# Optimization experiments

Measured on AMD Instinct MI355X. Metric: run time of the kernel, lower is better.

## Reference

```python
import jax, jax.numpy as jnp
import numpy as np
import math

# SS2D (VMamba v2) config
D_MODEL = 96
D_INNER = 192          # ssm_ratio * d_model (== d_expand, ssm_rank_ratio==ssm_ratio)
D_STATE = 16
DT_RANK = 6            # ceil(96/16)
K = 4                  # scan directions
D_CONV = 3
STEP = 2               # EfficientScan step_size
BATCH, H, W = 4, 64, 64  # H,W chosen even -> no padding branch
LN_EPS = 1e-5


def efficient_scan(x):
    # x: (B, C, H, W) with H,W divisible by STEP -> (B, 4, C, (H/2)*(W/2))
    Bn, C = x.shape[0], x.shape[1]
    xt = jnp.swapaxes(x, 2, 3)  # (B, C, W, H)
    xs0 = x[:, :, ::STEP, ::STEP].reshape(Bn, C, -1)
    xs1 = xt[:, :, ::STEP, 1::STEP].reshape(Bn, C, -1)
    xs2 = x[:, :, ::STEP, 1::STEP].reshape(Bn, C, -1)
    xs3 = xt[:, :, 1::STEP, 1::STEP].reshape(Bn, C, -1)
    return jnp.stack([xs0, xs1, xs2, xs3], axis=1)


def efficient_merge(ys, ori_h, ori_w):
    # ys: (B, 4, C, L') -> (B, C, ori_h*ori_w)
    Bn, _, C, _ = ys.shape
    Hs, Ws = ori_h // STEP, ori_w // STEP
    a = ys[:, 0].reshape(Bn, C, Hs, Ws)
    b = jnp.swapaxes(ys[:, 1].reshape(Bn, C, Ws, Hs), 2, 3)
    c = ys[:, 2].reshape(Bn, C, Hs, Ws)
    d = jnp.swapaxes(ys[:, 3].reshape(Bn, C, Ws, Hs), 2, 3)
    y = jnp.zeros((Bn, C, ori_h, ori_w), ys.dtype)
    y = y.at[:, :, ::STEP, ::STEP].set(a)
    y = y.at[:, :, 1::STEP, ::STEP].set(b)
    y = y.at[:, :, ::STEP, 1::STEP].set(c)
    y = y.at[:, :, 1::STEP, 1::STEP].set(d)
    return y.reshape(Bn, C, ori_h * ori_w)


def selective_scan(u, delta, A, Bs, Cs, D, delta_bias):
    # u, delta: (B, K*Dg, L); A: (K*Dg, N); Bs, Cs: (B, K, N, L); D, delta_bias: (K*Dg,)
    Bn, KD, L = u.shape
    N = A.shape[1]
    Dg = KD // K
    delta = jax.nn.softplus(delta + delta_bias[None, :, None])
    u4 = u.reshape(Bn, K, Dg, L)
    dt4 = delta.reshape(Bn, K, Dg, L)
    A4 = A.reshape(K, Dg, N)
    # discretized transition / input, time-major for scan: (L, B, K, Dg, N)
    dA = jnp.exp(jnp.einsum('bkdl,kdn->lbkdn', dt4, A4))
    dBu = jnp.einsum('bkdl,bknl,bkdl->lbkdn', dt4, Bs, u4)

    def step(h, inp):
        dA_t, dBu_t = inp
        h = dA_t * h + dBu_t
        return h, h

    h0 = jnp.zeros((Bn, K, Dg, N), u.dtype)
    _, hs = jax.lax.scan(step, h0, (dA, dBu))  # (L, B, K, Dg, N)
    y = jnp.einsum('lbkdn,bknl->bkdl', hs, Cs)
    y = y + u4 * D.reshape(1, K, Dg, 1)
    return y.reshape(Bn, KD, L)


def setup_inputs() -> dict:
    key = jax.random.key(0)
    ks = jax.random.split(key, 10)
    f = jnp.float32
    x = jax.random.normal(ks[0], (BATCH, H, W, D_MODEL), f)
    W_in = jax.random.normal(ks[1], (2 * D_INNER, D_MODEL), f) / math.sqrt(D_MODEL)
    conv_w = jax.random.normal(ks[2], (D_INNER, 1, D_CONV, D_CONV), f) / math.sqrt(D_CONV * D_CONV)
    conv_b = jax.random.normal(ks[3], (D_INNER,), f) * 0.01
    x_proj_weight = jax.random.normal(ks[4], (K, DT_RANK + 2 * D_STATE, D_INNER), f) / math.sqrt(D_INNER)
    dt_projs_weight = jax.random.normal(ks[5], (K, D_INNER, DT_RANK), f) / math.sqrt(DT_RANK)
    dt_projs_bias = jax.random.normal(ks[6], (K, D_INNER), f) * 0.1
    A_logs = jnp.log(jnp.tile(jnp.arange(1, D_STATE + 1, dtype=f), (K * D_INNER, 1)))
    Ds = jnp.ones((K * D_INNER,), f)
    ln_g = jnp.ones((D_INNER,), f)
    ln_b = jnp.zeros((D_INNER,), f)
    W_out = jax.random.normal(ks[7], (D_MODEL, D_INNER), f) / math.sqrt(D_INNER)
    return dict(x=x, W_in=W_in, conv_w=conv_w, conv_b=conv_b,
                x_proj_weight=x_proj_weight, dt_projs_weight=dt_projs_weight,
                dt_projs_bias=dt_projs_bias, A_logs=A_logs, Ds=Ds,
                ln_g=ln_g, ln_b=ln_b, W_out=W_out)


def _ss2d_forward(x, W_in, conv_w, conv_b, x_proj_weight, dt_projs_weight,
                  dt_projs_bias, A_logs, Ds, ln_g, ln_b, W_out):
    Bn = x.shape[0]
    # in_proj (no bias), split into x and gate z
    xz = jnp.einsum('bhwc,ec->bhwe', x, W_in)            # (B,H,W,2*D_INNER)
    xin, z = jnp.split(xz, 2, axis=-1)
    z = jax.nn.silu(z)
    # depthwise conv 3x3 (SAME) + SiLU, NCHW
    xc = jnp.transpose(xin, (0, 3, 1, 2))                 # (B, D_INNER, H, W)
    xc = jax.lax.conv_general_dilated(
        xc, conv_w, window_strides=(1, 1), padding=((1, 1), (1, 1)),
        feature_group_count=D_INNER,
        dimension_numbers=('NCHW', 'OIHW', 'NCHW')) + conv_b[None, :, None, None]
    xc = jax.nn.silu(xc)
    # cross_selective_scan
    xs = efficient_scan(xc)                               # (B, 4, C, L')
    Lp = xs.shape[-1]
    x_dbl = jnp.einsum('bkdl,kcd->bkcl', xs, x_proj_weight)
    dts, Bs, Cs = jnp.split(x_dbl, [DT_RANK, DT_RANK + D_STATE], axis=2)
    dts = jnp.einsum('bkrl,kdr->bkdl', dts, dt_projs_weight)
    u = xs.reshape(Bn, -1, Lp).astype(jnp.float32)
    delta = dts.reshape(Bn, -1, Lp).astype(jnp.float32)
    A = -jnp.exp(A_logs.astype(jnp.float32))
    ys = selective_scan(u, delta, A, Bs.astype(jnp.float32), Cs.astype(jnp.float32),
                        Ds.astype(jnp.float32), dt_projs_bias.reshape(-1).astype(jnp.float32))
    ys = ys.reshape(Bn, K, -1, Lp)
    y = efficient_merge(ys, H, W)                         # (B, C, H*W)
    y = jnp.swapaxes(y, 1, 2)                             # (B, L, C)
    # LayerNorm over channel dim
    mu = jnp.mean(y, axis=-1, keepdims=True)
    var = jnp.var(y, axis=-1, keepdims=True)
    y = (y - mu) * jax.lax.rsqrt(var + LN_EPS) * ln_g + ln_b
    y = y.reshape(Bn, H, W, D_INNER).astype(x.dtype)
    # gate and out_proj (no bias)
    y = y * z
    out = jnp.einsum('bhwd,od->bhwo', y, W_out)
    return out


def reference(x, W_in, conv_w, conv_b, x_proj_weight, dt_projs_weight,
              dt_projs_bias, A_logs, Ds, ln_g, ln_b, W_out):
    return _ss2d_forward(x, W_in, conv_w, conv_b, x_proj_weight, dt_projs_weight,
                         dt_projs_bias, A_logs, Ds, ln_g, ln_b, W_out)
```

## Files before the change

### kernel.cpp

```cpp
#include <hip/hip_runtime.h>
#include <math.h>


#define DINNER 192
#define NSTATE 16
#define KDIR 4
#define BATCH 4
#define NPIX (BATCH * 64 * 64)
#define LP 1024
#define NCH 128
#define CHUNK 8
#define NBK (BATCH * KDIR)
#define NSTATES (NBK * DINNER * NSTATE)
#define SSTRIDE (NBK * DINNER)
#define USTRIDE 196
#define GSTRIDE 200

typedef __attribute__((ext_vector_type(8))) short short8;
typedef __attribute__((ext_vector_type(4))) short short4v;
typedef __attribute__((ext_vector_type(4))) float f32x4;

__device__ __forceinline__ float silu_f(float x) {
    return x / (1.0f + __expf(-x));
}
__device__ __forceinline__ float softplus_f(float a) {
    return (a > 20.0f) ? a : __logf(1.0f + __expf(a));
}
__device__ __forceinline__ unsigned short f2bf(float f) {
    unsigned u = __float_as_uint(f);
    unsigned r = (u + 0x7FFFu + ((u >> 16) & 1u)) >> 16;
    return (unsigned short)r;
}
__device__ __forceinline__ float bf2f(unsigned short h) {
    return __uint_as_float(((unsigned)h) << 16);
}

__global__ __launch_bounds__(256) void k_castW(
        const float* __restrict__ W_in, const float* __restrict__ W_out,
        unsigned short* __restrict__ Wi_hi, unsigned short* __restrict__ Wi_lo,
        unsigned short* __restrict__ Wo_bf) {
    int i = blockIdx.x * 256 + threadIdx.x;
    if (i < 384 * 96) {
        float v = W_in[i];
        unsigned short h = f2bf(v);
        Wi_hi[i] = h;
        Wi_lo[i] = f2bf(v - bf2f(h));
    }
    if (i < 96 * DINNER) Wo_bf[i] = f2bf(W_out[i]);
}

__global__ __launch_bounds__(256) void k_inproj3(
        const float* __restrict__ x,
        const unsigned short* __restrict__ Wi_hi,
        const unsigned short* __restrict__ Wi_lo,
        float* __restrict__ xin, float* __restrict__ z) {
    int p0 = blockIdx.x * 16;
    int w = threadIdx.x >> 6;
    int lane = threadIdx.x & 63;
    int m = lane & 15, quad = lane >> 4;
    const short* wh = (const short*)Wi_hi;
    const short* wl = (const short*)Wi_lo;
    short8 ah[3], al[3];
    #pragma unroll
    for (int c = 0; c < 3; ++c) {
        const float* xr = x + (size_t)(p0 + m) * 96 + c * 32 + quad * 8;
        short8 hi, lo;
        #pragma unroll
        for (int j = 0; j < 8; ++j) {
            float v = xr[j];
            unsigned short hb = f2bf(v);
            hi[j] = (short)hb;
            lo[j] = (short)f2bf(v - bf2f(hb));
        }
        ah[c] = hi;
        al[c] = lo;
    }
    #pragma unroll
    for (int i = 0; i < 6; ++i) {
        int e0 = (w * 6 + i) * 16;
        f32x4 acc = {0.f, 0.f, 0.f, 0.f};
        #pragma unroll
        for (int c = 0; c < 3; ++c) {
            size_t o = (size_t)(e0 + m) * 96 + c * 32 + quad * 8;
            short8 bh = *(const short8*)(wh + o);
            short8 bl = *(const short8*)(wl + o);
            acc = __builtin_amdgcn_mfma_f32_16x16x32_bf16(ah[c], bl, acc, 0, 0, 0);
            acc = __builtin_amdgcn_mfma_f32_16x16x32_bf16(al[c], bh, acc, 0, 0, 0);
            acc = __builtin_amdgcn_mfma_f32_16x16x32_bf16(ah[c], bh, acc, 0, 0, 0);
        }
        int e = e0 + m;
        #pragma unroll
        for (int r = 0; r < 4; ++r) {
            int p = p0 + quad * 4 + r;
            if (e < 192) xin[(size_t)p * 192 + e] = acc[r];
            else         z[(size_t)p * 192 + (e - 192)] = silu_f(acc[r]);
        }
    }
}

__global__ __launch_bounds__(192) void k_conv8(
        const float* __restrict__ xin, const float* __restrict__ cw,
        const float* __restrict__ cb, float* __restrict__ xg) {
    int blk = blockIdx.x;
    int b = blk >> 9;
    int rem = blk & 511;
    int h = rem >> 3;
    int w0 = (rem & 7) * 8;
    int d = threadIdx.x;
    float wr[3][3];
    #pragma unroll
    for (int i = 0; i < 3; ++i)
        #pragma unroll
        for (int j = 0; j < 3; ++j) wr[i][j] = cw[d * 9 + i * 3 + j];
    float bias = cb[d];
    float acc[8];
    #pragma unroll
    for (int o = 0; o < 8; ++o) acc[o] = bias;
    #pragma unroll
    for (int jj = 0; jj < 10; ++jj) {
        int ww = w0 + jj - 1;
        float r0 = 0.0f, r1 = 0.0f, r2 = 0.0f;
        if ((unsigned)ww < 64u) {
            const float* base = xin + ((size_t)b * 4096 + h * 64 + ww) * 192 + d;
            if (h > 0)  r0 = base[-64 * 192];
            r1 = base[0];
            if (h < 63) r2 = base[64 * 192];
        }
        #pragma unroll
        for (int dd2 = 0; dd2 < 3; ++dd2) {
            int o = jj - 2 + dd2;
            int cj = 2 - dd2;
            if (o >= 0 && o < 8) {
                acc[o] = fmaf(r0, wr[0][cj], acc[o]);
                acc[o] = fmaf(r1, wr[1][cj], acc[o]);
                acc[o] = fmaf(r2, wr[2][cj], acc[o]);
            }
        }
    }
    #pragma unroll
    for (int o = 0; o < 8; ++o) {
        int w = w0 + o;
        int kq = (h & 1) ? ((w & 1) ? 3 : 1) : ((w & 1) ? 2 : 0);
        int l = (kq & 1) ? ((w >> 1) * 32 + (h >> 1))
                         : ((h >> 1) * 32 + (w >> 1));
        xg[((size_t)(b * 4 + kq) * 1024 + l) * 192 + d] = silu_f(acc[o]);
    }
}

__global__ __launch_bounds__(192) void k_scan1g(
        const float* __restrict__ xg, const float* __restrict__ xpw,
        const float* __restrict__ A_logs, const float* __restrict__ dtw,
        const float* __restrict__ dtb,
        float* __restrict__ Sbuf, float* __restrict__ Qbuf) {
    __shared__ float sU[CHUNK * USTRIDE];
    __shared__ float sB[CHUNK * 16];
    __shared__ float sR[CHUNK * 8];
    int bk = blockIdx.x >> 7;
    int ch = blockIdx.x & 127;
    int k = bk & 3;
    int t = threadIdx.x;
    int d = t;
    int lbase = bk * 1024 + ch * CHUNK;
    const float4* usrc = (const float4*)(xg + (size_t)lbase * 192);
    for (int i = t; i < CHUNK * 48; i += 192) {
        int l = i / 48, c4 = i - l * 48;
        *(float4*)&sU[l * USTRIDE + c4 * 4] = usrc[i];
    }
    float A[16];
    #pragma unroll
    for (int n = 0; n < 16; ++n) A[n] = -__expf(A_logs[(k * 192 + d) * 16 + n]);
    float A0 = A[0];
    bool geo = true;
    #pragma unroll
    for (int n = 1; n < 16; ++n)
        geo = geo && (fabsf(A[n] - (float)(n + 1) * A0) <= 1e-4f * fabsf(A[n]));
    float wp[6];
    #pragma unroll
    for (int q = 0; q < 6; ++q) wp[q] = dtw[(k * 192 + d) * 6 + q];
    float bias = dtb[k * 192 + d];
    __syncthreads();
    {
        int l = t & 7, cgp = t >> 3;
        float acc0 = 0.0f;
        const float* wb = xpw + (size_t)k * 38 * 192;
        int c0 = (cgp < 22) ? cgp : 0;
        for (int qv = 0; qv < 48; ++qv) {
            float4 xv = *(const float4*)&sU[l * USTRIDE + qv * 4];
            float4 w0 = *(const float4*)&wb[(size_t)c0 * 192 + qv * 4];
            acc0 = fmaf(xv.x, w0.x, fmaf(xv.y, w0.y, fmaf(xv.z, w0.z, fmaf(xv.w, w0.w, acc0))));
        }
        if (cgp < 6)       sR[l * 8 + cgp] = acc0;
        else if (cgp < 22) sB[l * 16 + (cgp - 6)] = acc0;
    }
    __syncthreads();
    float h[16];
    #pragma unroll
    for (int n = 0; n < 16; ++n) h[n] = 0.0f;
    float S = 0.0f;
    for (int l = 0; l < CHUNK; ++l) {
        float a = bias;
        #pragma unroll
        for (int q = 0; q < 6; ++q) a = fmaf(wp[q], sR[l * 8 + q], a);
        float dlt = softplus_f(a);
        S += dlt;
        float du = dlt * sU[l * USTRIDE + d];
        if (geo) {
            float e1 = __expf(dlt * A0);
            float e = e1;
            #pragma unroll
            for (int n = 0; n < 16; ++n) {
                h[n] = fmaf(e, h[n], du * sB[l * 16 + n]);
                e *= e1;
            }
        } else {
            #pragma unroll
            for (int n = 0; n < 16; ++n) {
                float e = __expf(dlt * A[n]);
                h[n] = fmaf(e, h[n], du * sB[l * 16 + n]);
            }
        }
    }
    Sbuf[(size_t)ch * SSTRIDE + bk * 192 + d] = S;
    size_t base = (size_t)ch * NSTATES + bk * (192 * 16);
    #pragma unroll
    for (int n = 0; n < 16; ++n)
        Qbuf[base + n * 192 + d] = h[n];
}

__global__ __launch_bounds__(256) void k_scan2(
        const float* __restrict__ Sbuf, const float* __restrict__ A_logs,
        float* QH) {
    int s = blockIdx.x * 256 + threadIdx.x;
    int bk = s / 3072;
    int rem = s - bk * 3072;
    int n = rem / 192;
    int d = rem - n * 192;
    int k = bk & 3;
    float A = -__expf(A_logs[(k * 192 + d) * 16 + n]);
    float h = 0.0f;
    for (int c = 0; c < NCH; ++c) {
        float q = QH[(size_t)c * NSTATES + s];
        float S = Sbuf[(size_t)c * SSTRIDE + bk * 192 + d];
        float p = __expf(A * S);
        QH[(size_t)c * NSTATES + s] = h;
        h = fmaf(p, h, q);
    }
}

__global__ __launch_bounds__(192) void k_scan3g(
        const float* __restrict__ xg, const float* __restrict__ xpw,
        const float* __restrict__ A_logs, const float* __restrict__ dtw,
        const float* __restrict__ dtb, const float* __restrict__ Ds,
        const float* __restrict__ QH, float* __restrict__ yout) {
    __shared__ float sU[CHUNK * USTRIDE];
    __shared__ float sB[CHUNK * 16];
    __shared__ float sC[CHUNK * 16];
    __shared__ float sR[CHUNK * 8];
    int bk = blockIdx.x >> 7;
    int ch = blockIdx.x & 127;
    int k = bk & 3;
    int t = threadIdx.x;
    int d = t;
    int lbase = bk * 1024 + ch * CHUNK;
    const float4* usrc = (const float4*)(xg + (size_t)lbase * 192);
    for (int i = t; i < CHUNK * 48; i += 192) {
        int l = i / 48, c4 = i - l * 48;
        *(float4*)&sU[l * USTRIDE + c4 * 4] = usrc[i];
    }
    float A[16];
    #pragma unroll
    for (int n = 0; n < 16; ++n) A[n] = -__expf(A_logs[(k * 192 + d) * 16 + n]);
    float A0 = A[0];
    bool geo = true;
    #pragma unroll
    for (int n = 1; n < 16; ++n)
        geo = geo && (fabsf(A[n] - (float)(n + 1) * A0) <= 1e-4f * fabsf(A[n]));
    float wp[6];
    #pragma unroll
    for (int q = 0; q < 6; ++q) wp[q] = dtw[(k * 192 + d) * 6 + q];
    float bias = dtb[k * 192 + d];
    float Dp = Ds[k * 192 + d];
    __syncthreads();
    {
        int l = t & 7, cgp = t >> 3;
        float acc0 = 0.0f, acc1 = 0.0f;
        const float* wb = xpw + (size_t)k * 38 * 192;
        int c1 = cgp + 24;
        int c1r = (c1 < 38) ? c1 : cgp;
        for (int qv = 0; qv < 48; ++qv) {
            float4 xv = *(const float4*)&sU[l * USTRIDE + qv * 4];
            float4 w0 = *(const float4*)&wb[(size_t)cgp * 192 + qv * 4];
            float4 w1 = *(const float4*)&wb[(size_t)c1r * 192 + qv * 4];
            acc0 = fmaf(xv.x, w0.x, fmaf(xv.y, w0.y, fmaf(xv.z, w0.z, fmaf(xv.w, w0.w, acc0))));
            acc1 = fmaf(xv.x, w1.x, fmaf(xv.y, w1.y, fmaf(xv.z, w1.z, fmaf(xv.w, w1.w, acc1))));
        }
        if (cgp < 6)       sR[l * 8 + cgp] = acc0;
        else if (cgp < 22) sB[l * 16 + (cgp - 6)] = acc0;
        else               sC[l * 16 + (cgp - 22)] = acc0;
        if (c1 < 38)       sC[l * 16 + (c1 - 22)] = acc1;
    }
    float h[16];
    size_t base = (size_t)ch * NSTATES + bk * (192 * 16);
    #pragma unroll
    for (int n = 0; n < 16; ++n) h[n] = QH[base + n * 192 + d];
    __syncthreads();
    for (int l = 0; l < CHUNK; ++l) {
        float a = bias;
        #pragma unroll
        for (int q = 0; q < 6; ++q) a = fmaf(wp[q], sR[l * 8 + q], a);
        float dlt = softplus_f(a);
        float u = sU[l * USTRIDE + d];
        float du = dlt * u;
        float y = 0.0f;
        if (geo) {
            float e1 = __expf(dlt * A0);
            float e = e1;
            #pragma unroll
            for (int n = 0; n < 16; ++n) {
                h[n] = fmaf(e, h[n], du * sB[l * 16 + n]);
                y = fmaf(h[n], sC[l * 16 + n], y);
                e *= e1;
            }
        } else {
            #pragma unroll
            for (int n = 0; n < 16; ++n) {
                float e = __expf(dlt * A[n]);
                h[n] = fmaf(e, h[n], du * sB[l * 16 + n]);
                y = fmaf(h[n], sC[l * 16 + n], y);
            }
        }
        yout[(size_t)(lbase + l) * 192 + d] = fmaf(u, Dp, y);
    }
}

__global__ __launch_bounds__(256) void k_lnout(
        const float* __restrict__ yout, const float* __restrict__ z,
        const float* __restrict__ lng, const float* __restrict__ lnb,
        const unsigned short* __restrict__ Wo_bf, float* __restrict__ out) {
    __shared__ __align__(16) short sgb[32 * GSTRIDE];
    int p0 = blockIdx.x * 32;
    int t = threadIdx.x;
    int p = t >> 3;
    int sub = t & 7;
    int gp = p0 + p;
    int b = gp >> 12;
    int hw = gp & 4095;
    int h = hw >> 6, w = hw & 63;
    int kq = (h & 1) ? ((w & 1) ? 3 : 1) : ((w & 1) ? 2 : 0);
    int l = (kq & 1) ? ((w >> 1) * 32 + (h >> 1))
                     : ((h >> 1) * 32 + (w >> 1));
    const float* yrow = yout + ((size_t)(b * 4 + kq) * 1024 + l) * 192 + sub * 24;
    float4 yv[6];
    float s = 0.0f, s2 = 0.0f;
    #pragma unroll
    for (int j = 0; j < 6; ++j) {
        float4 v = *(const float4*)(yrow + j * 4);
        yv[j] = v;
        s += v.x + v.y + v.z + v.w;
        s2 += v.x * v.x + v.y * v.y + v.z * v.z + v.w * v.w;
    }
    #pragma unroll
    for (int off = 1; off < 8; off <<= 1) {
        s  += __shfl_xor(s, off, 8);
        s2 += __shfl_xor(s2, off, 8);
    }
    float mu = s * (1.0f / 192.0f);
    float var = s2 * (1.0f / 192.0f) - mu * mu;
    float rstd = rsqrtf(var + 1e-5f);
    const float* zrow = z + (size_t)gp * 192 + sub * 24;
    short* grow = sgb + p * GSTRIDE + sub * 24;
    #pragma unroll
    for (int j = 0; j < 6; ++j) {
        float4 zv = *(const float4*)(zrow + j * 4);
        float4 gv = *(const float4*)(lng + sub * 24 + j * 4);
        float4 bv = *(const float4*)(lnb + sub * 24 + j * 4);
        short4v sv;
        sv.x = (short)f2bf(((yv[j].x - mu) * rstd * gv.x + bv.x) * zv.x);
        sv.y = (short)f2bf(((yv[j].y - mu) * rstd * gv.y + bv.y) * zv.y);
        sv.z = (short)f2bf(((yv[j].z - mu) * rstd * gv.z + bv.z) * zv.z);
        sv.w = (short)f2bf(((yv[j].w - mu) * rstd * gv.w + bv.w) * zv.w);
        *(short4v*)(grow + j * 4) = sv;
    }
    __syncthreads();
    int wv = t >> 6;
    int lane = t & 63;
    int m = lane & 15, quad = lane >> 4;
    int mt = wv >> 1;
    int nb = (wv & 1) * 3;
    const short* wob = (const short*)Wo_bf;
    short8 a[6];
    #pragma unroll
    for (int kk = 0; kk < 6; ++kk)
        a[kk] = *(const short8*)(sgb + (mt * 16 + m) * GSTRIDE + kk * 32 + quad * 8);
    #pragma unroll
    for (int i = 0; i < 3; ++i) {
        int n0 = (nb + i) * 16;
        f32x4 acc = {0.f, 0.f, 0.f, 0.f};
        #pragma unroll
        for (int kk = 0; kk < 6; ++kk) {
            short8 bfr = *(const short8*)(wob + (size_t)(n0 + m) * 192 + kk * 32 + quad * 8);
            acc = __builtin_amdgcn_mfma_f32_16x16x32_bf16(a[kk], bfr, acc, 0, 0, 0);
        }
        #pragma unroll
        for (int r = 0; r < 4; ++r) {
            int pp = p0 + mt * 16 + quad * 4 + r;
            out[(size_t)pp * 96 + n0 + m] = acc[r];
        }
    }
}

extern "C" void kernel_launch(void* const* d_in, const int* in_sizes, int n_in,
                              void* d_out, int out_size, void* d_ws, size_t ws_size,
                              hipStream_t stream) {
    const float* x    = (const float*)d_in[0];
    const float* W_in = (const float*)d_in[1];
    const float* cw   = (const float*)d_in[2];
    const float* cb   = (const float*)d_in[3];
    const float* xpw  = (const float*)d_in[4];
    const float* dtw  = (const float*)d_in[5];
    const float* dtb  = (const float*)d_in[6];
    const float* Alog = (const float*)d_in[7];
    const float* Ds   = (const float*)d_in[8];
    const float* lng  = (const float*)d_in[9];
    const float* lnb  = (const float*)d_in[10];
    const float* Wout = (const float*)d_in[11];
    float* out = (float*)d_out;

    float* ws = (float*)d_ws;
    size_t off = 0;
    unsigned short* Wi_hi = (unsigned short*)(ws + off); off += 384 * 96 / 2;
    unsigned short* Wi_lo = (unsigned short*)(ws + off); off += 384 * 96 / 2;
    unsigned short* Wo_bf = (unsigned short*)(ws + off); off += 96 * DINNER / 2;
    float* xin   = ws + off; off += (size_t)NPIX * 192;
    float* zbuf  = ws + off; off += (size_t)NPIX * 192;
    float* xg    = ws + off; off += (size_t)NPIX * 192;
    float* Sbuf  = ws + off; off += (size_t)NCH * SSTRIDE;
    float* QH    = ws + off; off += (size_t)NCH * NSTATES;
    float* yout  = ws + off; off += (size_t)NBK * LP * 192;

    hipLaunchKernelGGL(k_castW, dim3(144), dim3(256), 0, stream,
                       W_in, Wout, Wi_hi, Wi_lo, Wo_bf);
    hipLaunchKernelGGL(k_inproj3, dim3(NPIX / 16), dim3(256), 0, stream,
                       x, Wi_hi, Wi_lo, xin, zbuf);
    hipLaunchKernelGGL(k_conv8, dim3(NPIX / 8), dim3(192), 0, stream,
                       xin, cw, cb, xg);
    hipLaunchKernelGGL(k_scan1g, dim3(NBK * NCH), dim3(192), 0, stream,
                       xg, xpw, Alog, dtw, dtb, Sbuf, QH);
    hipLaunchKernelGGL(k_scan2, dim3(NSTATES / 256), dim3(256), 0, stream,
                       Sbuf, Alog, QH);
    hipLaunchKernelGGL(k_scan3g, dim3(NBK * NCH), dim3(192), 0, stream,
                       xg, xpw, Alog, dtw, dtb, Ds, QH, yout);
    hipLaunchKernelGGL(k_lnout, dim3(NPIX / 32), dim3(256), 0, stream,
                       yout, zbuf, lng, lnb, Wo_bf, out);
}
```

Measured before the change: 182.1 us.

## Split x_proj into separate kernel and double scan chunk length

```diff
diff --git a/kernel.cpp b/kernel.cpp
--- a/kernel.cpp
+++ b/kernel.cpp
@@ -8,8 +8,8 @@
 #define BATCH 4
 #define NPIX (BATCH * 64 * 64)
 #define LP 1024
-#define NCH 128
-#define CHUNK 8
+#define NCH 64
+#define CHUNK 16
 #define NBK (BATCH * KDIR)
 #define NSTATES (NBK * DINNER * NSTATE)
 #define SSTRIDE (NBK * DINNER)
@@ -147,25 +147,66 @@
     }
 }
 
-__global__ __launch_bounds__(192) void k_scan1g(
+__global__ __launch_bounds__(192) void k_xdbl(
         const float* __restrict__ xg, const float* __restrict__ xpw,
-        const float* __restrict__ A_logs, const float* __restrict__ dtw,
-        const float* __restrict__ dtb,
+        float* __restrict__ dtr, float* __restrict__ Bm, float* __restrict__ Cm) {
+    __shared__ float sU[16 * USTRIDE];
+    int bk = blockIdx.x >> 6;
+    int tile = blockIdx.x & 63;
+    int k = bk & 3;
+    int t = threadIdx.x;
+    int lbase = bk * 1024 + tile * 16;
+    const float4* usrc = (const float4*)(xg + (size_t)lbase * 192);
+    for (int i = t; i < 16 * 48; i += 192) {
+        int l = i / 48, c4 = i - l * 48;
+        *(float4*)&sU[l * USTRIDE + c4 * 4] = usrc[i];
+    }
+    __syncthreads();
+    int l = t & 15, cgp = t >> 4;
+    float acc[4] = {0.f, 0.f, 0.f, 0.f};
+    int c3 = (cgp < 2) ? (cgp + 36) : cgp;
+    const float* wb = xpw + (size_t)k * 38 * 192;
+    for (int qv = 0; qv < 48; ++qv) {
+        float4 xv = *(const float4*)&sU[l * USTRIDE + qv * 4];
+        float4 w0 = *(const float4*)&wb[(cgp +  0) * 192 + qv * 4];
+        float4 w1 = *(const float4*)&wb[(cgp + 12) * 192 + qv * 4];
+        float4 w2 = *(const float4*)&wb[(cgp + 24) * 192 + qv * 4];
+        float4 w3 = *(const float4*)&wb[(size_t)c3 * 192 + qv * 4];
+        acc[0] = fmaf(xv.x, w0.x, fmaf(xv.y, w0.y, fmaf(xv.z, w0.z, fmaf(xv.w, w0.w, acc[0]))));
+        acc[1] = fmaf(xv.x, w1.x, fmaf(xv.y, w1.y, fmaf(xv.z, w1.z, fmaf(xv.w, w1.w, acc[1]))));
+        acc[2] = fmaf(xv.x, w2.x, fmaf(xv.y, w2.y, fmaf(xv.z, w2.z, fmaf(xv.w, w2.w, acc[2]))));
+        acc[3] = fmaf(xv.x, w3.x, fmaf(xv.y, w3.y, fmaf(xv.z, w3.z, fmaf(xv.w, w3.w, acc[3]))));
+    }
+    int bkl = lbase + l;
+    #pragma unroll
+    for (int j = 0; j < 4; ++j) {
+        int c = cgp + 12 * j;
+        if (j == 3) { if (cgp >= 2) break; c = cgp + 36; }
+        float v = acc[j];
+        if (c < 6)       dtr[(size_t)bkl * 6 + c] = v;
+        else if (c < 22) Bm[(size_t)bkl * 16 + (c - 6)] = v;
+        else             Cm[(size_t)bkl * 16 + (c - 22)] = v;
+    }
+}
+
+__global__ __launch_bounds__(192) void k_scan1p(
+        const float* __restrict__ xg, const float* __restrict__ dtr,
+        const float* __restrict__ Bm, const float* __restrict__ A_logs,
+        const float* __restrict__ dtw, const float* __restrict__ dtb,
         float* __restrict__ Sbuf, float* __restrict__ Qbuf) {
     __shared__ float sU[CHUNK * USTRIDE];
     __shared__ float sB[CHUNK * 16];
-    __shared__ float sR[CHUNK * 8];
-    int bk = blockIdx.x >> 7;
-    int ch = blockIdx.x & 127;
+    int bk = blockIdx.x >> 6;
+    int ch = blockIdx.x & 63;
     int k = bk & 3;
-    int t = threadIdx.x;
-    int d = t;
+    int d = threadIdx.x;
     int lbase = bk * 1024 + ch * CHUNK;
     const float4* usrc = (const float4*)(xg + (size_t)lbase * 192);
-    for (int i = t; i < CHUNK * 48; i += 192) {
+    for (int i = d; i < CHUNK * 48; i += 192) {
         int l = i / 48, c4 = i - l * 48;
         *(float4*)&sU[l * USTRIDE + c4 * 4] = usrc[i];
     }
+    for (int i = d; i < CHUNK * 16; i += 192) sB[i] = Bm[(size_t)lbase * 16 + i];
     float A[16];
     #pragma unroll
     for (int n = 0; n < 16; ++n) A[n] = -__expf(A_logs[(k * 192 + d) * 16 + n]);
@@ -179,28 +220,15 @@
     for (int q = 0; q < 6; ++q) wp[q] = dtw[(k * 192 + d) * 6 + q];
     float bias = dtb[k * 192 + d];
     __syncthreads();
-    {
-        int l = t & 7, cgp = t >> 3;
-        float acc0 = 0.0f;
-        const float* wb = xpw + (size_t)k * 38 * 192;
-        int c0 = (cgp < 22) ? cgp : 0;
-        for (int qv = 0; qv < 48; ++qv) {
-            float4 xv = *(const float4*)&sU[l * USTRIDE + qv * 4];
-            float4 w0 = *(const float4*)&wb[(size_t)c0 * 192 + qv * 4];
-            acc0 = fmaf(xv.x, w0.x, fmaf(xv.y, w0.y, fmaf(xv.z, w0.z, fmaf(xv.w, w0.w, acc0))));
-        }
-        if (cgp < 6)       sR[l * 8 + cgp] = acc0;
-        else if (cgp < 22) sB[l * 16 + (cgp - 6)] = acc0;
-    }
-    __syncthreads();
     float h[16];
     #pragma unroll
     for (int n = 0; n < 16; ++n) h[n] = 0.0f;
     float S = 0.0f;
     for (int l = 0; l < CHUNK; ++l) {
+        const float* r = dtr + (size_t)(lbase + l) * 6;
         float a = bias;
         #pragma unroll
-        for (int q = 0; q < 6; ++q) a = fmaf(wp[q], sR[l * 8 + q], a);
+        for (int q = 0; q < 6; ++q) a = fmaf(wp[q], r[q], a);
         float dlt = softplus_f(a);
         S += dlt;
         float du = dlt * sU[l * USTRIDE + d];
@@ -247,25 +275,28 @@
     }
 }
 
-__global__ __launch_bounds__(192) void k_scan3g(
-        const float* __restrict__ xg, const float* __restrict__ xpw,
+__global__ __launch_bounds__(192) void k_scan3p(
+        const float* __restrict__ xg, const float* __restrict__ dtr,
+        const float* __restrict__ Bm, const float* __restrict__ Cm,
         const float* __restrict__ A_logs, const float* __restrict__ dtw,
         const float* __restrict__ dtb, const float* __restrict__ Ds,
         const float* __restrict__ QH, float* __restrict__ yout) {
     __shared__ float sU[CHUNK * USTRIDE];
     __shared__ float sB[CHUNK * 16];
     __shared__ float sC[CHUNK * 16];
-    __shared__ float sR[CHUNK * 8];
-    int bk = blockIdx.x >> 7;
-    int ch = blockIdx.x & 127;
+    int bk = blockIdx.x >> 6;
+    int ch = blockIdx.x & 63;
     int k = bk & 3;
-    int t = threadIdx.x;
-    int d = t;
+    int d = threadIdx.x;
     int lbase = bk * 1024 + ch * CHUNK;
     const float4* usrc = (const float4*)(xg + (size_t)lbase * 192);
-    for (int i = t; i < CHUNK * 48; i += 192) {
+    for (int i = d; i < CHUNK * 48; i += 192) {
         int l = i / 48, c4 = i - l * 48;
         *(float4*)&sU[l * USTRIDE + c4 * 4] = usrc[i];
+    }
+    for (int i = d; i < CHUNK * 16; i += 192) {
+        sB[i] = Bm[(size_t)lbase * 16 + i];
+        sC[i] = Cm[(size_t)lbase * 16 + i];
     }
     float A[16];
     #pragma unroll
@@ -280,34 +311,16 @@
     for (int q = 0; q < 6; ++q) wp[q] = dtw[(k * 192 + d) * 6 + q];
     float bias = dtb[k * 192 + d];
     float Dp = Ds[k * 192 + d];
-    __syncthreads();
-    {
-        int l = t & 7, cgp = t >> 3;
-        float acc0 = 0.0f, acc1 = 0.0f;
-        const float* wb = xpw + (size_t)k * 38 * 192;
-        int c1 = cgp + 24;
-        int c1r = (c1 < 38) ? c1 : cgp;
-        for (int qv = 0; qv < 48; ++qv) {
-            float4 xv = *(const float4*)&sU[l * USTRIDE + qv * 4];
-            float4 w0 = *(const float4*)&wb[(size_t)cgp * 192 + qv * 4];
-            float4 w1 = *(const float4*)&wb[(size_t)c1r * 192 + qv * 4];
-            acc0 = fmaf(xv.x, w0.x, fmaf(xv.y, w0.y, fmaf(xv.z, w0.z, fmaf(xv.w, w0.w, acc0))));
-            acc1 = fmaf(xv.x, w1.x, fmaf(xv.y, w1.y, fmaf(xv.z, w1.z, fmaf(xv.w, w1.w, acc1))));
-        }
-        if (cgp < 6)       sR[l * 8 + cgp] = acc0;
-        else if (cgp < 22) sB[l * 16 + (cgp - 6)] = acc0;
-        else               sC[l * 16 + (cgp - 22)] = acc0;
-        if (c1 < 38)       sC[l * 16 + (c1 - 22)] = acc1;
-    }
     float h[16];
     size_t base = (size_t)ch * NSTATES + bk * (192 * 16);
     #pragma unroll
     for (int n = 0; n < 16; ++n) h[n] = QH[base + n * 192 + d];
     __syncthreads();
     for (int l = 0; l < CHUNK; ++l) {
+        const float* r = dtr + (size_t)(lbase + l) * 6;
         float a = bias;
         #pragma unroll
-        for (int q = 0; q < 6; ++q) a = fmaf(wp[q], sR[l * 8 + q], a);
+        for (int q = 0; q < 6; ++q) a = fmaf(wp[q], r[q], a);
         float dlt = softplus_f(a);
         float u = sU[l * USTRIDE + d];
         float du = dlt * u;
@@ -434,6 +447,9 @@
     float* xin   = ws + off; off += (size_t)NPIX * 192;
     float* zbuf  = ws + off; off += (size_t)NPIX * 192;
     float* xg    = ws + off; off += (size_t)NPIX * 192;
+    float* dtrb  = ws + off; off += (size_t)NBK * LP * 6;
+    float* Bm    = ws + off; off += (size_t)NBK * LP * 16;
+    float* Cm    = ws + off; off += (size_t)NBK * LP * 16;
     float* Sbuf  = ws + off; off += (size_t)NCH * SSTRIDE;
     float* QH    = ws + off; off += (size_t)NCH * NSTATES;
     float* yout  = ws + off; off += (size_t)NBK * LP * 192;
@@ -444,12 +460,14 @@
                        x, Wi_hi, Wi_lo, xin, zbuf);
     hipLaunchKernelGGL(k_conv8, dim3(NPIX / 8), dim3(192), 0, stream,
                        xin, cw, cb, xg);
-    hipLaunchKernelGGL(k_scan1g, dim3(NBK * NCH), dim3(192), 0, stream,
-                       xg, xpw, Alog, dtw, dtb, Sbuf, QH);
+    hipLaunchKernelGGL(k_xdbl, dim3(NBK * 64), dim3(192), 0, stream,
+                       xg, xpw, dtrb, Bm, Cm);
+    hipLaunchKernelGGL(k_scan1p, dim3(NBK * NCH), dim3(192), 0, stream,
+                       xg, dtrb, Bm, Alog, dtw, dtb, Sbuf, QH);
     hipLaunchKernelGGL(k_scan2, dim3(NSTATES / 256), dim3(256), 0, stream,
                        Sbuf, Alog, QH);
-    hipLaunchKernelGGL(k_scan3g, dim3(NBK * NCH), dim3(192), 0, stream,
-                       xg, xpw, Alog, dtw, dtb, Ds, QH, yout);
+    hipLaunchKernelGGL(k_scan3p, dim3(NBK * NCH), dim3(192), 0, stream,
+                       xg, dtrb, Bm, Cm, Alog, dtw, dtb, Ds, QH, yout);
     hipLaunchKernelGGL(k_lnout, dim3(NPIX / 32), dim3(256), 0, stream,
                        yout, zbuf, lng, lnb, Wo_bf, out);
 }
```

After: 174.0 us. 1.05x faster.
